# Optimization experiments

Measured on AMD Instinct MI355X. Metric: run time of the kernel, lower is better.

Reference implementation:

```python
import jax, jax.numpy as jnp
import numpy as np

VOCAB, F, H1, H2 = 64, 4096, 64, 32   # vocab size, featureVectorSize, hidden dims (hard-coded 64/32/1 in source)
NBBOX, NWORDS = 8192, 16


def _uniform(key, shape, fan_in):
    # torch nn.Linear default init: U(-1/sqrt(fan_in), 1/sqrt(fan_in))
    bound = 1.0 / np.sqrt(fan_in)
    return jax.random.uniform(key, shape, jnp.float32, -bound, bound)


def setup_inputs() -> dict:
    key = jax.random.key(0)
    ks = jax.random.split(key, 8)
    x = jax.random.normal(ks[0], (NBBOX, F), jnp.float32)
    words = jax.random.randint(ks[1], (NWORDS,), 0, VOCAB)  # indices of active word-models
    # Stacked per-word MLP params (one tiny MLP per vocab word)
    W1 = _uniform(ks[2], (VOCAB, F, H1), F)
    b1 = _uniform(ks[3], (VOCAB, H1), F)
    W2 = _uniform(ks[4], (VOCAB, H1, H2), H1)
    b2 = _uniform(ks[5], (VOCAB, H2), H1)
    W3 = _uniform(ks[6], (VOCAB, H2), H2)   # Linear(32,1) weight, squeezed to [VOCAB, H2]
    b3 = _uniform(ks[7], (VOCAB,), H2)
    return {"nBBox": NBBOX, "x": x, "words": words,
            "W1": W1, "b1": b1, "W2": W2, "b2": b2, "W3": W3, "b3": b3}


def reference(nBBox, x, words, W1, b1, W2, b2, W3, b3):
    # Gather the active word-models (dict lookup in the original)
    w1, c1 = W1[words], b1[words]          # [W,F,H1], [W,H1]
    w2, c2 = W2[words], b2[words]          # [W,H1,H2], [W,H2]
    w3, c3 = W3[words], b3[words]          # [W,H2], [W]
    # Batched 3-layer MLP over all active words at once (replaces Python loop)
    h1 = jax.nn.relu(jnp.einsum('bf,wfh->wbh', x, w1) + c1[:, None, :])   # [W,B,H1]
    h2 = jax.nn.relu(jnp.einsum('wbh,whk->wbk', h1, w2) + c2[:, None, :])  # [W,B,H2]
    logits = jnp.einsum('wbk,wk->wb', h2, w3) + c3[:, None]                # [W,B]
    # output = ones(nBBox,1) * prod_w sigmoid(logits_w)
    return jnp.prod(jax.nn.sigmoid(logits), axis=0)[:, None]               # [B,1]
```

## Files before the change

### kernel.cpp

```cpp
#include <hip/hip_runtime.h>
#include <stdint.h>
#include <math.h>

#define NBBOX 8192
#define FDIM  4096
#define H1DIM 64
#define H2DIM 32
#define NW    16
#define NCOL  1024

typedef __attribute__((ext_vector_type(8))) _Float16 f16x8;
typedef __attribute__((ext_vector_type(4))) float    f32x4;

typedef __attribute__((address_space(1))) void* gptr_t;
typedef __attribute__((address_space(3))) void* lptr_t;

__device__ __forceinline__ void g2l16(const void* g, void* l) {
    __builtin_amdgcn_global_load_lds((gptr_t)(uintptr_t)g,
                                     (lptr_t)(uint32_t)(uintptr_t)l,
                                     16, 0, 0);
}

__global__ void convert_x(const float* __restrict__ x, _Float16* __restrict__ xh) {
    int gid = blockIdx.x * blockDim.x + threadIdx.x;
    int idx = gid * 8;
    float4 a = *(const float4*)(x + idx);
    float4 b = *(const float4*)(x + idx + 4);
    f16x8 h;
    h[0] = (_Float16)a.x; h[1] = (_Float16)a.y; h[2] = (_Float16)a.z; h[3] = (_Float16)a.w;
    h[4] = (_Float16)b.x; h[5] = (_Float16)b.y; h[6] = (_Float16)b.z; h[7] = (_Float16)b.w;
    *(f16x8*)(xh + idx) = h;
}

__global__ __launch_bounds__(256) void gather_w(
    const float* __restrict__ W1, const int* __restrict__ words,
    uint32_t* __restrict__ bth_u32)
{
    __shared__ uint32_t t[64 * 69];
    const int wi = blockIdx.x >> 5;
    const int ft = blockIdx.x & 31;
    const int f0 = ft * 128;
    const int w  = words[wi];
    const int tid  = threadIdx.x;
    const int c    = tid & 63;
    const int fgrp = tid >> 6;

    const float* src = W1 + ((size_t)w * FDIM + f0) * H1DIM + c;
#pragma unroll
    for (int p = 0; p < 16; ++p) {
        const int f = fgrp * 2 + p * 8;
        float v0 = src[(size_t)f * H1DIM];
        float v1 = src[(size_t)(f + 1) * H1DIM];
        union { _Float16 h[2]; uint32_t u; } pk;
        pk.h[0] = (_Float16)v0; pk.h[1] = (_Float16)v1;
        t[c * 69 + (f >> 1)] = pk.u;
    }
    __syncthreads();
#pragma unroll
    for (int p = 0; p < 16; ++p) {
        const int cc = p * 4 + (tid >> 6);
        const int fd = tid & 63;
        bth_u32[(size_t)(wi * 64 + cc) * (FDIM / 2) + ft * 64 + fd] = t[cc * 69 + fd];
    }
}

__global__ __launch_bounds__(256, 2) void gemm_l1(
    const _Float16* __restrict__ xh, const _Float16* __restrict__ bth,
    const float* __restrict__ b1, const int* __restrict__ words,
    float* __restrict__ Hout)
{
    __shared__ _Float16 As[2][128 * 32];
    __shared__ _Float16 Bs[2][128 * 32];

    const int mt   = blockIdx.x >> 3;
    const int nt   = blockIdx.x & 7;
    const int t    = threadIdx.x;
    const int w    = t >> 6;
    const int lane = t & 63;
    const int m0 = mt * 128, n0 = nt * 128;

    f32x4 acc[4][4] = {};

    const int rs = w * 16 + (lane >> 2);
    const int kc = (lane & 3) * 8;

    const _Float16* A = xh  + (size_t)m0 * FDIM;
    const _Float16* B = bth + (size_t)n0 * FDIM;

    const int wm = w >> 1, wn = w & 1;
    const int ml = lane & 15;
    const int q8 = (lane >> 4) * 8;

    for (int kt = 0; kt < 64; ++kt) {
        const int k0 = kt * 64;
#pragma unroll
        for (int s = 0; s < 2; ++s) {
            const int kp = k0 + s * 32 + kc;
            g2l16(A + (size_t)rs * FDIM + kp,        &As[s][w * 512]);
            g2l16(A + (size_t)(rs + 64) * FDIM + kp, &As[s][2048 + w * 512]);
            g2l16(B + (size_t)rs * FDIM + kp,        &Bs[s][w * 512]);
            g2l16(B + (size_t)(rs + 64) * FDIM + kp, &Bs[s][2048 + w * 512]);
        }
        __syncthreads();

#pragma unroll
        for (int s = 0; s < 2; ++s) {
            f16x8 af[4], bfr[4];
#pragma unroll
            for (int i = 0; i < 4; ++i)
                af[i] = *(const f16x8*)&As[s][(wm * 64 + i * 16 + ml) * 32 + q8];
#pragma unroll
            for (int j = 0; j < 4; ++j)
                bfr[j] = *(const f16x8*)&Bs[s][(wn * 64 + j * 16 + ml) * 32 + q8];
#pragma unroll
            for (int i = 0; i < 4; ++i)
#pragma unroll
                for (int j = 0; j < 4; ++j)
                    acc[i][j] = __builtin_amdgcn_mfma_f32_16x16x32_f16(af[i], bfr[j], acc[i][j], 0, 0, 0);
        }
        __syncthreads();
    }

    const int q = lane >> 4;
#pragma unroll
    for (int j = 0; j < 4; ++j) {
        const int gcol = n0 + wn * 64 + j * 16 + ml;
        const float bias = b1[words[gcol >> 6] * H1DIM + (gcol & 63)];
#pragma unroll
        for (int i = 0; i < 4; ++i) {
            const int grow0 = m0 + wm * 64 + i * 16 + q * 4;
#pragma unroll
            for (int r = 0; r < 4; ++r) {
                float v = acc[i][j][r] + bias;
                Hout[(size_t)(grow0 + r) * NCOL + gcol] = v > 0.f ? v : 0.f;
            }
        }
    }
}

__global__ __launch_bounds__(256) void tail_mlp(
    const float* __restrict__ Hbuf, const int* __restrict__ words,
    const float* __restrict__ W2, const float* __restrict__ b2,
    const float* __restrict__ W3, const float* __restrict__ b3,
    float* __restrict__ sig)
{
    __shared__ float tile[4][64 * 64];
    const int t    = threadIdx.x;
    const int v    = t >> 6;
    const int lane = t & 63;
    const int wi   = blockIdx.x >> 5;
    const int rb   = blockIdx.x & 31;
    const int r0   = rb * 256 + v * 64;
    const int wv   = words[wi];

    {
        const int rr = lane >> 4;
        const int kch = lane & 15;
#pragma unroll
        for (int p = 0; p < 16; ++p) {
            const int row = p * 4 + rr;
            float4 d = *(const float4*)&Hbuf[(size_t)(r0 + row) * NCOL + wi * H1DIM + kch * 4];
            const int pos = ((kch + row) & 7) | (kch & 8);
            *(float4*)&tile[v][row * 64 + pos * 4] = d;
        }
    }

    const float* W2w = W2 + (size_t)wv * (H1DIM * H2DIM);
    float acc[H2DIM];
#pragma unroll
    for (int j = 0; j < H2DIM; ++j) acc[j] = 0.f;

#pragma unroll
    for (int c = 0; c < 16; ++c) {
        const int pos = ((c + lane) & 7) | (c & 8);
        f32x4 h = *(const f32x4*)&tile[v][lane * 64 + pos * 4];
#pragma unroll
        for (int kk = 0; kk < 4; ++kk) {
            const float hv = h[kk];
            const int k = c * 4 + kk;
#pragma unroll
            for (int j = 0; j < H2DIM; ++j)
                acc[j] = fmaf(hv, W2w[k * H2DIM + j], acc[j]);
        }
    }

    float logit = b3[wv];
#pragma unroll
    for (int j = 0; j < H2DIM; ++j) {
        float h2 = acc[j] + b2[wv * H2DIM + j];
        h2 = h2 > 0.f ? h2 : 0.f;
        logit = fmaf(h2, W3[wv * H2DIM + j], logit);
    }
    sig[(size_t)wi * NBBOX + r0 + lane] = 1.f / (1.f + expf(-logit));
}

__global__ void prod_k(const float* __restrict__ sig, float* __restrict__ out) {
    const int r = blockIdx.x * 256 + threadIdx.x;
    float p = 1.f;
#pragma unroll
    for (int wi = 0; wi < NW; ++wi) p *= sig[(size_t)wi * NBBOX + r];
    out[r] = p;
}

extern "C" void kernel_launch(void* const* d_in, const int* in_sizes, int n_in,
                              void* d_out, int out_size, void* d_ws, size_t ws_size,
                              hipStream_t stream)
{
    const float* x   = (const float*)d_in[1];
    const int* words = (const int*)  d_in[2];
    const float* W1  = (const float*)d_in[3];
    const float* b1  = (const float*)d_in[4];
    const float* W2  = (const float*)d_in[5];
    const float* b2  = (const float*)d_in[6];
    const float* W3  = (const float*)d_in[7];
    const float* b3  = (const float*)d_in[8];
    float* out = (float*)d_out;

    char* ws = (char*)d_ws;
    _Float16* xh  = (_Float16*)(ws);
    _Float16* bth = (_Float16*)(ws + 67108864);
    float*    Hb  = (float*)   (ws + 67108864 + 8388608);
    float*    sig = (float*)   (ws);

    convert_x<<<NBBOX * FDIM / 8 / 256, 256, 0, stream>>>(x, xh);
    gather_w<<<512, 256, 0, stream>>>(W1, words, (uint32_t*)bth);
    gemm_l1<<<512, 256, 0, stream>>>(xh, bth, b1, words, Hb);
    tail_mlp<<<512, 256, 0, stream>>>(Hb, words, W2, b2, W3, b3, sig);
    prod_k<<<NBBOX / 256, 256, 0, stream>>>(sig, out);
}
```

Before: 341.7 us.

## Fuse tail MLP into GEMM epilogue, double-buffer GEMM loads, merge prep kernels

Merges the x conversion and the W1 gather into one launch. The layer-2/3 MLP is moved into the GEMM epilogue, so the 32MB hidden activation buffer is no longer written and read back through global memory; each wave stages its 64x64 ReLU tile in LDS with an XOR swizzle. The GEMM main loop is double-buffered so next-tile global-to-LDS loads overlap MFMA compute. LDS use doubles to 64KB, which may limit occupancy, and the fused epilogue adds register pressure.

```diff
diff --git a/kernel.cpp b/kernel.cpp
--- a/kernel.cpp
+++ b/kernel.cpp
@@ -21,22 +21,23 @@
                                      16, 0, 0);
 }
 
-__global__ void convert_x(const float* __restrict__ x, _Float16* __restrict__ xh) {
-    int gid = blockIdx.x * blockDim.x + threadIdx.x;
-    int idx = gid * 8;
-    float4 a = *(const float4*)(x + idx);
-    float4 b = *(const float4*)(x + idx + 4);
-    f16x8 h;
-    h[0] = (_Float16)a.x; h[1] = (_Float16)a.y; h[2] = (_Float16)a.z; h[3] = (_Float16)a.w;
-    h[4] = (_Float16)b.x; h[5] = (_Float16)b.y; h[6] = (_Float16)b.z; h[7] = (_Float16)b.w;
-    *(f16x8*)(xh + idx) = h;
-}
-
-__global__ __launch_bounds__(256) void gather_w(
+__global__ __launch_bounds__(256) void prep(
+    const float* __restrict__ x, _Float16* __restrict__ xh,
     const float* __restrict__ W1, const int* __restrict__ words,
     uint32_t* __restrict__ bth_u32)
 {
     __shared__ uint32_t t[64 * 69];
+    if (blockIdx.x >= 512) {
+        int gid = (blockIdx.x - 512) * 256 + threadIdx.x;
+        int idx = gid * 8;
+        float4 a = *(const float4*)(x + idx);
+        float4 b = *(const float4*)(x + idx + 4);
+        f16x8 h;
+        h[0] = (_Float16)a.x; h[1] = (_Float16)a.y; h[2] = (_Float16)a.z; h[3] = (_Float16)a.w;
+        h[4] = (_Float16)b.x; h[5] = (_Float16)b.y; h[6] = (_Float16)b.z; h[7] = (_Float16)b.w;
+        *(f16x8*)(xh + idx) = h;
+        return;
+    }
     const int wi = blockIdx.x >> 5;
     const int ft = blockIdx.x & 31;
     const int f0 = ft * 128;
@@ -64,13 +65,14 @@
     }
 }
 
-__global__ __launch_bounds__(256, 2) void gemm_l1(
+__global__ __launch_bounds__(256, 2) void gemm_fused(
     const _Float16* __restrict__ xh, const _Float16* __restrict__ bth,
-    const float* __restrict__ b1, const int* __restrict__ words,
-    float* __restrict__ Hout)
+    const int* __restrict__ words, const float* __restrict__ b1,
+    const float* __restrict__ W2, const float* __restrict__ b2,
+    const float* __restrict__ W3, const float* __restrict__ b3,
+    float* __restrict__ sig)
 {
-    __shared__ _Float16 As[2][128 * 32];
-    __shared__ _Float16 Bs[2][128 * 32];
+    __shared__ __align__(16) _Float16 smem[32768];
 
     const int mt   = blockIdx.x >> 3;
     const int nt   = blockIdx.x & 7;
@@ -91,107 +93,92 @@
     const int ml = lane & 15;
     const int q8 = (lane >> 4) * 8;
 
+    auto stage = [&](int b, int k0) {
+#pragma unroll
+        for (int s = 0; s < 2; ++s) {
+            _Float16* Ap = smem + (b * 2 + s) * 4096;
+            _Float16* Bp = smem + 16384 + (b * 2 + s) * 4096;
+            const int kp = k0 + s * 32 + kc;
+            g2l16(A + (size_t)rs * FDIM + kp,        Ap + w * 512);
+            g2l16(A + (size_t)(rs + 64) * FDIM + kp, Ap + 2048 + w * 512);
+            g2l16(B + (size_t)rs * FDIM + kp,        Bp + w * 512);
+            g2l16(B + (size_t)(rs + 64) * FDIM + kp, Bp + 2048 + w * 512);
+        }
+    };
+
+    stage(0, 0);
     for (int kt = 0; kt < 64; ++kt) {
-        const int k0 = kt * 64;
+        const int b = kt & 1;
+        __syncthreads();
+        if (kt < 63) stage(b ^ 1, (kt + 1) * 64);
 #pragma unroll
         for (int s = 0; s < 2; ++s) {
-            const int kp = k0 + s * 32 + kc;
-            g2l16(A + (size_t)rs * FDIM + kp,        &As[s][w * 512]);
-            g2l16(A + (size_t)(rs + 64) * FDIM + kp, &As[s][2048 + w * 512]);
-            g2l16(B + (size_t)rs * FDIM + kp,        &Bs[s][w * 512]);
-            g2l16(B + (size_t)(rs + 64) * FDIM + kp, &Bs[s][2048 + w * 512]);
-        }
-        __syncthreads();
-
-#pragma unroll
-        for (int s = 0; s < 2; ++s) {
+            const _Float16* Ap = smem + (b * 2 + s) * 4096;
+            const _Float16* Bp = smem + 16384 + (b * 2 + s) * 4096;
             f16x8 af[4], bfr[4];
 #pragma unroll
             for (int i = 0; i < 4; ++i)
-                af[i] = *(const f16x8*)&As[s][(wm * 64 + i * 16 + ml) * 32 + q8];
+                af[i] = *(const f16x8*)&Ap[(wm * 64 + i * 16 + ml) * 32 + q8];
 #pragma unroll
             for (int j = 0; j < 4; ++j)
-                bfr[j] = *(const f16x8*)&Bs[s][(wn * 64 + j * 16 + ml) * 32 + q8];
+                bfr[j] = *(const f16x8*)&Bp[(wn * 64 + j * 16 + ml) * 32 + q8];
 #pragma unroll
             for (int i = 0; i < 4; ++i)
 #pragma unroll
                 for (int j = 0; j < 4; ++j)
                     acc[i][j] = __builtin_amdgcn_mfma_f32_16x16x32_f16(af[i], bfr[j], acc[i][j], 0, 0, 0);
         }
-        __syncthreads();
-    }
+    }
+    __syncthreads();
+
+    const int word = nt * 2 + wn;
+    const int wv   = words[word];
+    float* tilef = (float*)smem + w * 4096;
 
     const int q = lane >> 4;
 #pragma unroll
     for (int j = 0; j < 4; ++j) {
-        const int gcol = n0 + wn * 64 + j * 16 + ml;
-        const float bias = b1[words[gcol >> 6] * H1DIM + (gcol & 63)];
-#pragma unroll
-        for (int i = 0; i < 4; ++i) {
-            const int grow0 = m0 + wm * 64 + i * 16 + q * 4;
+        const float bias = b1[wv * H1DIM + j * 16 + ml];
+#pragma unroll
+        for (int i = 0; i < 4; ++i)
 #pragma unroll
             for (int r = 0; r < 4; ++r) {
                 float v = acc[i][j][r] + bias;
-                Hout[(size_t)(grow0 + r) * NCOL + gcol] = v > 0.f ? v : 0.f;
+                v = v > 0.f ? v : 0.f;
+                const int row   = i * 16 + q * 4 + r;
+                const int chunk = j * 4 + (ml >> 2);
+                const int phys  = chunk ^ (row & 15);
+                tilef[row * 64 + phys * 4 + (ml & 3)] = v;
             }
-        }
-    }
-}
-
-__global__ __launch_bounds__(256) void tail_mlp(
-    const float* __restrict__ Hbuf, const int* __restrict__ words,
-    const float* __restrict__ W2, const float* __restrict__ b2,
-    const float* __restrict__ W3, const float* __restrict__ b3,
-    float* __restrict__ sig)
-{
-    __shared__ float tile[4][64 * 64];
-    const int t    = threadIdx.x;
-    const int v    = t >> 6;
-    const int lane = t & 63;
-    const int wi   = blockIdx.x >> 5;
-    const int rb   = blockIdx.x & 31;
-    const int r0   = rb * 256 + v * 64;
-    const int wv   = words[wi];
-
-    {
-        const int rr = lane >> 4;
-        const int kch = lane & 15;
-#pragma unroll
-        for (int p = 0; p < 16; ++p) {
-            const int row = p * 4 + rr;
-            float4 d = *(const float4*)&Hbuf[(size_t)(r0 + row) * NCOL + wi * H1DIM + kch * 4];
-            const int pos = ((kch + row) & 7) | (kch & 8);
-            *(float4*)&tile[v][row * 64 + pos * 4] = d;
-        }
     }
 
     const float* W2w = W2 + (size_t)wv * (H1DIM * H2DIM);
-    float acc[H2DIM];
-#pragma unroll
-    for (int j = 0; j < H2DIM; ++j) acc[j] = 0.f;
+    float acc2[H2DIM];
+#pragma unroll
+    for (int j = 0; j < H2DIM; ++j) acc2[j] = 0.f;
 
 #pragma unroll
     for (int c = 0; c < 16; ++c) {
-        const int pos = ((c + lane) & 7) | (c & 8);
-        f32x4 h = *(const f32x4*)&tile[v][lane * 64 + pos * 4];
+        const int phys = c ^ (lane & 15);
+        f32x4 h = *(const f32x4*)&tilef[lane * 64 + phys * 4];
 #pragma unroll
         for (int kk = 0; kk < 4; ++kk) {
             const float hv = h[kk];
             const int k = c * 4 + kk;
 #pragma unroll
             for (int j = 0; j < H2DIM; ++j)
-                acc[j] = fmaf(hv, W2w[k * H2DIM + j], acc[j]);
+                acc2[j] = fmaf(hv, W2w[k * H2DIM + j], acc2[j]);
         }
     }
 
     float logit = b3[wv];
 #pragma unroll
     for (int j = 0; j < H2DIM; ++j) {
-        float h2 = acc[j] + b2[wv * H2DIM + j];
+        float h2 = acc2[j] + b2[wv * H2DIM + j];
         h2 = h2 > 0.f ? h2 : 0.f;
         logit = fmaf(h2, W3[wv * H2DIM + j], logit);
     }
-    sig[(size_t)wi * NBBOX + r0 + lane] = 1.f / (1.f + expf(-logit));
+    sig[(size_t)word * NBBOX + m0 + wm * 64 + lane] = 1.f / (1.f + expf(-logit));
 }
 
 __global__ void prod_k(const float* __restrict__ sig, float* __restrict__ out) {
@@ -219,12 +206,9 @@
     char* ws = (char*)d_ws;
     _Float16* xh  = (_Float16*)(ws);
     _Float16* bth = (_Float16*)(ws + 67108864);
-    float*    Hb  = (float*)   (ws + 67108864 + 8388608);
-    float*    sig = (float*)   (ws);
-
-    convert_x<<<NBBOX * FDIM / 8 / 256, 256, 0, stream>>>(x, xh);
-    gather_w<<<512, 256, 0, stream>>>(W1, words, (uint32_t*)bth);
-    gemm_l1<<<512, 256, 0, stream>>>(xh, bth, b1, words, Hb);
-    tail_mlp<<<512, 256, 0, stream>>>(Hb, words, W2, b2, W3, b3, sig);
+    float*    sig = (float*)   (ws + 67108864 + 8388608);
+
+    prep<<<512 + NBBOX * FDIM / 8 / 256, 256, 0, stream>>>(x, xh, W1, words, (uint32_t*)bth);
+    gemm_fused<<<512, 256, 0, stream>>>(xh, bth, words, b1, W2, b2, W3, b3, sig);
     prod_k<<<NBBOX / 256, 256, 0, stream>>>(sig, out);
 }
```

Measured after the change: 344.8 us. Within noise of the previous version (+0.9%).
